# Kernel tuning notes

Measured on AMD Instinct MI355X. Metric: run time of the kernel, lower is better.

The kernel has to match this reference:

```python
import jax, jax.numpy as jnp
import numpy as np

H = 16      # num_heads
HD = 64     # head_dim
W = 1024    # local window size
G = 256     # number of global tokens
EPS = 1e-6
NEG = -1e30


def setup_inputs() -> dict:
    key = jax.random.key(0)
    ks = jax.random.split(key, 7)
    B, S, D = 1, 8192, 1024
    inner = H * HD
    s = 0.02
    return {
        "x": jax.random.normal(ks[0], (B, S, D), jnp.float32),
        "norm_w": jnp.ones((D,), jnp.float32),
        "w_q": jax.random.normal(ks[1], (D, inner), jnp.float32) * s,
        "w_k": jax.random.normal(ks[2], (D, inner), jnp.float32) * s,
        "w_v": jax.random.normal(ks[3], (D, inner), jnp.float32) * s,
        "w_out": jax.random.normal(ks[4], (inner, D), jnp.float32) * s,
        "scorer_w": jax.random.normal(ks[5], (D, 1), jnp.float32) * s,
        "scorer_b": jnp.zeros((1,), jnp.float32),
    }


def reference(x, norm_w, w_q, w_k, w_v, w_out, scorer_w, scorer_b):
    B, S, D = x.shape
    # pre-norm (RMSNorm)
    h = x * jax.lax.rsqrt(jnp.mean(x * x, axis=-1, keepdims=True) + EPS) * norm_w

    def proj(w):  # [B,S,D] -> [B,H,S,HD]
        return jnp.einsum('bsd,de->bse', h, w).reshape(B, S, H, HD).transpose(0, 2, 1, 3)

    q, k, v = proj(w_q), proj(w_k), proj(w_v)
    scale = HD ** -0.5

    # --- local block attention (non-overlapping causal windows) ---
    nW = S // W
    qw = q.reshape(B, H, nW, W, HD)
    kw = k.reshape(B, H, nW, W, HD)
    vw = v.reshape(B, H, nW, W, HD)
    ll = jnp.einsum('bhnqd,bhnkd->bhnqk', qw, kw) * scale  # [B,H,nW,W,W]
    cm = jnp.tril(jnp.ones((W, W), bool))
    ll = jnp.where(cm, ll, NEG).reshape(B, H, S, W)

    # --- sparse global attention over top-G important tokens ---
    scores = (jnp.einsum('bsd,do->bso', h, scorer_w) + scorer_b)[..., 0]  # [B,S]
    _, idx = jax.lax.top_k(scores, G)                                     # [B,G]
    kg = jnp.take_along_axis(k, idx[:, None, :, None], axis=2)            # [B,H,G,HD]
    vg = jnp.take_along_axis(v, idx[:, None, :, None], axis=2)
    lg = jnp.einsum('bhsd,bhgd->bhsg', q, kg) * scale                     # [B,H,S,G]
    pos = jnp.arange(S)
    gmask = idx[:, None, None, :] <= pos[None, None, :, None]             # causal: global pos <= query pos
    lg = jnp.where(gmask, lg, NEG)

    # --- joint softmax over local window + global tokens ---
    attn = jax.nn.softmax(jnp.concatenate([ll, lg], axis=-1), axis=-1)    # [B,H,S,W+G]
    a_loc = attn[..., :W].reshape(B, H, nW, W, W)
    o = jnp.einsum('bhnqk,bhnkd->bhnqd', a_loc, vw).reshape(B, H, S, HD)
    o = o + jnp.einsum('bhsg,bhgd->bhsd', attn[..., W:], vg)

    o = o.transpose(0, 2, 1, 3).reshape(B, S, H * HD)
    return x + jnp.einsum('bse,ed->bsd', o, w_out)  # residual
```

## Files before the change

### kernel.cpp

```cpp
#include <hip/hip_runtime.h>
#include <stdint.h>

#define S_LEN 8192
#define DIM   1024
#define NH    16
#define HD    64
#define WIN   1024
#define GTOK  256
#define QKV_STRIDE (3 * DIM)

typedef __attribute__((ext_vector_type(8))) short bf16x8;
typedef __attribute__((ext_vector_type(4))) float f32x4;
typedef __attribute__((ext_vector_type(16))) float f32x16;
typedef unsigned short u16;
typedef uint32_t u32;

__device__ __forceinline__ u16 f2bf(float f) {
  union { float f; uint32_t u; } v; v.f = f;
  uint32_t r = v.u + 0x7fffu + ((v.u >> 16) & 1u);
  return (u16)(r >> 16);
}
__device__ __forceinline__ float bf2f(u16 b) {
  union { uint32_t u; float f; } v; v.u = ((uint32_t)b) << 16;
  return v.f;
}
__device__ __forceinline__ uint32_t cvtpk(float a, float b) {
  uint32_t r;
  asm("v_cvt_pk_bf16_f32 %0, %1, %2" : "=v"(r) : "v"(a), "v"(b));
  return r;
}

__device__ __forceinline__ void gload_lds16(const void* g, void* l) {
  __builtin_amdgcn_global_load_lds((const __attribute__((address_space(1))) void*)g,
                                   (__attribute__((address_space(3))) void*)l, 16, 0, 0);
}

__global__ __launch_bounds__(256) void rmsnorm_score_kernel(
    const float* __restrict__ x, const float* __restrict__ nw,
    const float* __restrict__ sw, const float* __restrict__ sb,
    u16* __restrict__ h, float* __restrict__ scores) {
  int row = blockIdx.x, tid = threadIdx.x;
  const float4* xr = (const float4*)(x + (size_t)row * DIM);
  float4 v = xr[tid];
  float ss = v.x * v.x + v.y * v.y + v.z * v.z + v.w * v.w;
#pragma unroll
  for (int o = 32; o >= 1; o >>= 1) ss += __shfl_xor(ss, o);
  __shared__ float red[4], red2[4];
  int wv = tid >> 6;
  if ((tid & 63) == 0) red[wv] = ss;
  __syncthreads();
  ss = red[0] + red[1] + red[2] + red[3];
  float rn = rsqrtf(ss * (1.0f / DIM) + 1e-6f);
  float4 w4 = ((const float4*)nw)[tid];
  float h0 = v.x * rn * w4.x, h1 = v.y * rn * w4.y;
  float h2 = v.z * rn * w4.z, h3 = v.w * rn * w4.w;
  uint64_t pack = (uint64_t)f2bf(h0) | ((uint64_t)f2bf(h1) << 16) |
                  ((uint64_t)f2bf(h2) << 32) | ((uint64_t)f2bf(h3) << 48);
  *(uint64_t*)(h + (size_t)row * DIM + tid * 4) = pack;
  float4 s4 = ((const float4*)sw)[tid];
  float sc = h0 * s4.x + h1 * s4.y + h2 * s4.z + h3 * s4.w;
#pragma unroll
  for (int o = 32; o >= 1; o >>= 1) sc += __shfl_xor(sc, o);
  if ((tid & 63) == 0) red2[wv] = sc;
  __syncthreads();
  if (tid == 0) scores[row] = red2[0] + red2[1] + red2[2] + red2[3] + sb[0];
}

__global__ __launch_bounds__(256) void transpose_w_kernel(
    const float* __restrict__ wq, const float* __restrict__ wk,
    const float* __restrict__ wv, const float* __restrict__ wo,
    u16* __restrict__ wqkvT, u16* __restrict__ woutT) {
  __shared__ float tile[32][33];
  int z = blockIdx.z;
  const float* src = (z == 0) ? wq : (z == 1) ? wk : (z == 2) ? wv : wo;
  u16* dst = (z < 3) ? (wqkvT + (size_t)z * DIM * DIM) : woutT;
  int tx = threadIdx.x, ty = threadIdx.y;
  int n0 = blockIdx.x * 32, k0 = blockIdx.y * 32;
#pragma unroll
  for (int i = 0; i < 4; i++)
    tile[ty + i * 8][tx] = src[(size_t)(k0 + ty + i * 8) * DIM + n0 + tx];
  __syncthreads();
#pragma unroll
  for (int i = 0; i < 4; i++)
    dst[(size_t)(n0 + ty + i * 8) * DIM + k0 + tx] = f2bf(tile[tx][ty + i * 8]);
}

__global__ __launch_bounds__(256) void topk_init_kernel(int* __restrict__ cnt) {
  cnt[blockIdx.x * 256 + threadIdx.x] = 0;
}

__global__ __launch_bounds__(256) void topk_count_kernel(
    const float* __restrict__ scores, int* __restrict__ cnt) {
  __shared__ float sj[1024];
  int jbase = blockIdx.y * 1024;
  for (int t = threadIdx.x; t < 1024; t += 256) sj[t] = scores[jbase + t];
  __syncthreads();
  int i = blockIdx.x * 256 + threadIdx.x;
  float my = scores[i];
  int c = 0;
  const float4* s4 = (const float4*)sj;
#pragma unroll 4
  for (int j = 0; j < 256; j++) {
    float4 v = s4[j];
    int b = jbase + j * 4;
    c += (v.x > my) || (v.x == my && (b + 0) < i);
    c += (v.y > my) || (v.y == my && (b + 1) < i);
    c += (v.z > my) || (v.z == my && (b + 2) < i);
    c += (v.w > my) || (v.w == my && (b + 3) < i);
  }
  if (c) atomicAdd(&cnt[i], c);
}

__global__ __launch_bounds__(256) void topk_scatter_kernel(
    const int* __restrict__ cnt, int* __restrict__ gidx) {
  int i = blockIdx.x * 256 + threadIdx.x;
  int c = cnt[i];
  if (c < GTOK) gidx[c] = i;
}

__global__ __launch_bounds__(128) void gather_kernel(
    const u16* __restrict__ qkv, const int* __restrict__ gidx,
    u16* __restrict__ kg, u16* __restrict__ vg) {
  int g = blockIdx.x, t = threadIdx.x;
  size_t src = (size_t)gidx[g] * QKV_STRIDE;
  *(bf16x8*)(kg + (size_t)g * DIM + t * 8) = *(const bf16x8*)(qkv + src + DIM + t * 8);
  *(bf16x8*)(vg + (size_t)g * DIM + t * 8) = *(const bf16x8*)(qkv + src + 2 * DIM + t * 8);
}

template <int RESID>
__global__ __launch_bounds__(512, 2) void gemm256_kernel(
    const u16* __restrict__ A, const u16* __restrict__ B,
    u16* __restrict__ Cb, float* __restrict__ Cf, const float* __restrict__ X,
    int M, int N, int K) {
  __shared__ __align__(16) u16 As[3][256 * 64];
  __shared__ __align__(16) u16 Bs[3][128 * 64];
  const int tid = threadIdx.x;
  const int wave = tid >> 6, lane = tid & 63;
  const int l15 = lane & 15, l4 = lane >> 4;
  const int wr = wave >> 1, wc = wave & 1;
  const int mbase = blockIdx.x * 256, nbase = blockIdx.y * 128;
  const int srow = lane >> 3, schunk = lane & 7;
  const int gcol = (schunk ^ srow) * 8;

  auto stage = [&](int tt, int b) {
    const int kt = tt << 6;
#pragma unroll
    for (int l = 0; l < 4; l++) {
      int row = wave * 32 + l * 8;
      gload_lds16(A + (size_t)(mbase + row + srow) * K + kt + gcol, &As[b][row * 64]);
    }
#pragma unroll
    for (int l = 0; l < 2; l++) {
      int row = wave * 16 + l * 8;
      gload_lds16(B + (size_t)(nbase + row + srow) * K + kt + gcol, &Bs[b][row * 64]);
    }
  };

  const int nt = K >> 6;
  f32x4 acc[4][4] = {};

  stage(0, 0);
  stage(1, 1);
  asm volatile("s_waitcnt vmcnt(6)" ::: "memory");
  __builtin_amdgcn_s_barrier();
  __builtin_amdgcn_sched_barrier(0);

  int cur = 0;
  for (int t = 0; t < nt; t++) {
    int pre = cur + 2; if (pre >= 3) pre -= 3;
    if (t + 2 < nt) stage(t + 2, pre);
    const u16* Ab = &As[cur][0];
    const u16* Bb = &Bs[cur][0];
    bf16x8 bfr[4][2], af[4][2];
#pragma unroll
    for (int nf = 0; nf < 4; nf++) {
      int row = wc * 64 + nf * 16 + l15;
#pragma unroll
      for (int kk = 0; kk < 2; kk++)
        bfr[nf][kk] = *(const bf16x8*)(Bb + row * 64 + (((kk * 4 + l4) ^ (l15 & 7)) * 8));
    }
#pragma unroll
    for (int mi = 0; mi < 4; mi++) {
      int row = wr * 64 + mi * 16 + l15;
#pragma unroll
      for (int kk = 0; kk < 2; kk++)
        af[mi][kk] = *(const bf16x8*)(Ab + row * 64 + (((kk * 4 + l4) ^ (l15 & 7)) * 8));
    }
    __builtin_amdgcn_s_setprio(1);
#pragma unroll
    for (int mi = 0; mi < 4; mi++)
#pragma unroll
      for (int nf = 0; nf < 4; nf++)
#pragma unroll
        for (int kk = 0; kk < 2; kk++)
          acc[mi][nf] = __builtin_amdgcn_mfma_f32_16x16x32_bf16(af[mi][kk], bfr[nf][kk],
                                                                acc[mi][nf], 0, 0, 0);
    __builtin_amdgcn_s_setprio(0);
    if (t + 1 < nt) {
      if (t + 2 < nt) asm volatile("s_waitcnt vmcnt(6)" ::: "memory");
      else            asm volatile("s_waitcnt vmcnt(0)" ::: "memory");
      __builtin_amdgcn_s_barrier();
      __builtin_amdgcn_sched_barrier(0);
    }
    cur = (cur + 1 == 3) ? 0 : cur + 1;
  }

#pragma unroll
  for (int mi = 0; mi < 4; mi++) {
#pragma unroll
    for (int nf = 0; nf < 4; nf++) {
#pragma unroll
      for (int r = 0; r < 4; r++) {
        int row = mbase + wr * 64 + mi * 16 + l4 * 4 + r;
        int col = nbase + wc * 64 + nf * 16 + l15;
        float v = acc[mi][nf][r];
        if (RESID) Cf[(size_t)row * N + col] = X[(size_t)row * N + col] + v;
        else       Cb[(size_t)row * N + col] = f2bf(v);
      }
    }
  }
}

__global__ __launch_bounds__(256) void attn_kernel(
    const u16* __restrict__ qkv, const u16* __restrict__ kg,
    const u16* __restrict__ vg, const int* __restrict__ gidx,
    u16* __restrict__ o) {
  __shared__ __align__(16) u16 kT[2][64][72];
  __shared__ __align__(16) u16 vT[2][64][72];
  __shared__ int gposLds[2][64];
  const int tid = threadIdx.x, wave = tid >> 6, lane = tid & 63;
  const int l31 = lane & 31, hi = lane >> 5;
  const int win = blockIdx.x >> 2, pr = blockIdx.x & 3;
  const int wbase = win * WIN;
  const int hoff = blockIdx.y * HD;
  const int ks = (l31 >> 3) & 3;

  const int skey = tid >> 2;
  const int kc0 = (tid & 3) * 2;
  const int kswz = (skey >> 3) & 3;
  const int kp = tid & 31, dblk = tid >> 5;
  const int vcol = kp ^ ((dblk & 3) << 2);

  bf16x8 nk0, nk1, nva, nvb;
  int ng = 0;
  {
    const u16* kb = qkv + (size_t)(wbase + skey) * QKV_STRIDE + DIM + hoff;
    nk0 = *(const bf16x8*)(kb + kc0 * 8);
    nk1 = *(const bf16x8*)(kb + kc0 * 8 + 8);
    const u16* vb = qkv + (size_t)(wbase + 2 * kp) * QKV_STRIDE + 2 * DIM + hoff + dblk * 8;
    nva = *(const bf16x8*)(vb);
    nvb = *(const bf16x8*)(vb + QKV_STRIDE);
  }

  for (int sp = 0; sp < 2; sp++) {
    const int j = sp ? (7 - pr) : pr;
    const int qsbase = wbase + j * 128;
    const int nLocal = (j + 1) * 2;
    const int nTiles = nLocal + GTOK / 64;
    const int qrow = qsbase + wave * 32 + l31;
    const int qwmax = qsbase + wave * 32 + 31;

    bf16x8 qf[4];
    {
      const float SC2 = 0.125f * 1.44269504088896f;
      const u16* qptr = qkv + (size_t)qrow * QKV_STRIDE + hoff + hi * 8;
#pragma unroll
      for (int ksub = 0; ksub < 4; ksub++) {
        bf16x8 raw = *(const bf16x8*)(qptr + ksub * 16);
        bf16x8 sc;
#pragma unroll
        for (int jj = 0; jj < 8; jj++) sc[jj] = (short)f2bf(bf2f((u16)raw[jj]) * SC2);
        qf[ksub] = sc;
      }
    }

    f32x16 acc0 = {}, acc1 = {};
    float mr = -3.0e38f, lr = 0.f;

    __syncthreads();

    for (int t = 0; t < nTiles; t++) {
      const int p = t & 1;
      const bool isLocal = (t < nLocal);
      const int tbase = wbase + t * 64;
      *(bf16x8*)(&kT[p][skey][(kc0 ^ kswz) * 8]) = nk0;
      *(bf16x8*)(&kT[p][skey][((kc0 + 1) ^ kswz) * 8]) = nk1;
#pragma unroll
      for (int jj = 0; jj < 8; jj++) {
        uint32_t pk2 = (u16)nva[jj] | ((uint32_t)(u16)nvb[jj] << 16);
        ((u32*)&vT[p][dblk * 8 + jj][0])[vcol] = pk2;
      }
      if (!isLocal && tid < 64) gposLds[p][tid] = ng;
      {
        const int ntile = t + 1;
        const u16 *ksrc = nullptr, *vsrc = nullptr;
        size_t vstride = QKV_STRIDE;
        if (ntile < nLocal) {
          ksrc = qkv + (size_t)(wbase + ntile * 64 + skey) * QKV_STRIDE + DIM + hoff + kc0 * 8;
          vsrc = qkv + (size_t)(wbase + ntile * 64 + 2 * kp) * QKV_STRIDE + 2 * DIM + hoff + dblk * 8;
        } else if (ntile < nTiles) {
          ksrc = kg + (size_t)((ntile - nLocal) * 64 + skey) * DIM + hoff + kc0 * 8;
          vsrc = vg + (size_t)((ntile - nLocal) * 64 + 2 * kp) * DIM + hoff + dblk * 8;
          vstride = DIM;
          if (tid < 64) ng = gidx[(ntile - nLocal) * 64 + tid];
        } else if (sp == 0) {
          ksrc = qkv + (size_t)(wbase + skey) * QKV_STRIDE + DIM + hoff + kc0 * 8;
          vsrc = qkv + (size_t)(wbase + 2 * kp) * QKV_STRIDE + 2 * DIM + hoff + dblk * 8;
        }
        if (ksrc) {
          nk0 = *(const bf16x8*)(ksrc);
          nk1 = *(const bf16x8*)(ksrc + 8);
          nva = *(const bf16x8*)(vsrc);
          nvb = *(const bf16x8*)(vsrc + vstride);
        }
      }
      asm volatile("s_waitcnt lgkmcnt(0)" ::: "memory");
      __builtin_amdgcn_s_barrier();
      __builtin_amdgcn_sched_barrier(0);

      if (isLocal && tbase > qwmax) continue;

      float sv[32];
      __builtin_amdgcn_s_setprio(1);
#pragma unroll
      for (int kb = 0; kb < 2; kb++) {
        const u16* krow = &kT[p][kb * 32 + l31][0];
        bf16x8 k0 = *(const bf16x8*)(krow + ((hi + 0) ^ ks) * 8);
        bf16x8 k1 = *(const bf16x8*)(krow + ((hi + 2) ^ ks) * 8);
        bf16x8 k2 = *(const bf16x8*)(krow + ((hi + 4) ^ ks) * 8);
        bf16x8 k3 = *(const bf16x8*)(krow + ((hi + 6) ^ ks) * 8);
        f32x16 z = {};
        z = __builtin_amdgcn_mfma_f32_32x32x16_bf16(k0, qf[0], z, 0, 0, 0);
        z = __builtin_amdgcn_mfma_f32_32x32x16_bf16(k1, qf[1], z, 0, 0, 0);
        z = __builtin_amdgcn_mfma_f32_32x32x16_bf16(k2, qf[2], z, 0, 0, 0);
        z = __builtin_amdgcn_mfma_f32_32x32x16_bf16(k3, qf[3], z, 0, 0, 0);
#pragma unroll
        for (int r = 0; r < 16; r++) sv[kb * 16 + r] = z[r];
      }
      __builtin_amdgcn_s_setprio(0);

      if (isLocal) {
        const int lim = qrow - tbase;
        if (lim < 63) {
#pragma unroll
          for (int kb = 0; kb < 2; kb++)
#pragma unroll
            for (int r = 0; r < 16; r++) {
              int crow = kb * 32 + (r & 3) + 8 * (r >> 2) + 4 * hi;
              if (crow > lim) sv[kb * 16 + r] = -3.0e38f;
            }
        }
      } else {
#pragma unroll
        for (int kb = 0; kb < 2; kb++)
#pragma unroll
          for (int r = 0; r < 16; r++) {
            int kpos = gposLds[p][kb * 32 + (r & 3) + 8 * (r >> 2) + 4 * hi];
            if (kpos > qrow) sv[kb * 16 + r] = -3.0e38f;
          }
      }

      float m0 = sv[0], m1 = sv[1], m2 = sv[2], m3 = sv[3];
#pragma unroll
      for (int i = 4; i < 32; i += 4) {
        m0 = fmaxf(m0, sv[i]);     m1 = fmaxf(m1, sv[i + 1]);
        m2 = fmaxf(m2, sv[i + 2]); m3 = fmaxf(m3, sv[i + 3]);
      }
      float vmax = fmaxf(fmaxf(m0, m1), fmaxf(m2, m3));
      vmax = fmaxf(vmax, __shfl_xor(vmax, 32));
      if (__any(vmax > mr + 11.0f)) {
        float mn = fmaxf(mr, vmax);
        float al = exp2f(mr - mn);
        lr *= al;
        mr = mn;
#pragma unroll
        for (int i = 0; i < 16; i++) { acc0[i] *= al; acc1[i] *= al; }
      }
      float s0 = 0.f, s1 = 0.f, s2 = 0.f, s3 = 0.f;
#pragma unroll
      for (int i = 0; i < 32; i += 4) {
        float p0 = exp2f(sv[i] - mr),     p1 = exp2f(sv[i + 1] - mr);
        float p2 = exp2f(sv[i + 2] - mr), p3 = exp2f(sv[i + 3] - mr);
        sv[i] = p0; sv[i + 1] = p1; sv[i + 2] = p2; sv[i + 3] = p3;
        s0 += p0; s1 += p1; s2 += p2; s3 += p3;
      }
      float ps = (s0 + s1) + (s2 + s3);
      ps += __shfl_xor(ps, 32);
      lr += ps;

      bf16x8 pf[4];
#pragma unroll
      for (int q4 = 0; q4 < 4; q4++) {
        int b = q4 * 8;
        uint32_t w0 = cvtpk(sv[b + 0], sv[b + 1]);
        uint32_t w1 = cvtpk(sv[b + 2], sv[b + 3]);
        uint32_t w2 = cvtpk(sv[b + 4], sv[b + 5]);
        uint32_t w3 = cvtpk(sv[b + 6], sv[b + 7]);
        uint32_t w0s = __shfl_xor((int)w0, 32), w2s = __shfl_xor((int)w2, 32);
        uint32_t w1s = __shfl_xor((int)w1, 32), w3s = __shfl_xor((int)w3, 32);
        union { uint32_t w[4]; bf16x8 v; } u;
        u.w[0] = hi ? w2s : w0;
        u.w[1] = hi ? w3s : w1;
        u.w[2] = hi ? w2 : w0s;
        u.w[3] = hi ? w3 : w1s;
        pf[q4] = u.v;
      }

      __builtin_amdgcn_s_setprio(1);
#pragma unroll
      for (int dsel = 0; dsel < 2; dsel++) {
        const u16* vrow = &vT[p][dsel * 32 + l31][0];
        f32x16 a = dsel ? acc1 : acc0;
#pragma unroll
        for (int ksg = 0; ksg < 4; ksg++) {
          bf16x8 vf = *(const bf16x8*)(vrow + (((ksg * 2 + hi) ^ ks) * 8));
          a = __builtin_amdgcn_mfma_f32_32x32x16_bf16(vf, pf[ksg], a, 0, 0, 0);
        }
        if (dsel) acc1 = a; else acc0 = a;
      }
      __builtin_amdgcn_s_setprio(0);
    }

    float inv = 1.0f / lr;
#pragma unroll
    for (int dsel = 0; dsel < 2; dsel++) {
      f32x16 a = dsel ? acc1 : acc0;
#pragma unroll
      for (int g = 0; g < 4; g++) {
        uint64_t pk = (uint64_t)f2bf(a[g * 4 + 0] * inv)
                    | ((uint64_t)f2bf(a[g * 4 + 1] * inv) << 16)
                    | ((uint64_t)f2bf(a[g * 4 + 2] * inv) << 32)
                    | ((uint64_t)f2bf(a[g * 4 + 3] * inv) << 48);
        *(uint64_t*)(o + (size_t)qrow * DIM + hoff + dsel * 32 + g * 8 + 4 * hi) = pk;
      }
    }
  }
}

extern "C" void kernel_launch(void* const* d_in, const int* in_sizes, int n_in,
                              void* d_out, int out_size, void* d_ws, size_t ws_size,
                              hipStream_t stream) {
  const float* x  = (const float*)d_in[0];
  const float* nw = (const float*)d_in[1];
  const float* wq = (const float*)d_in[2];
  const float* wk = (const float*)d_in[3];
  const float* wv = (const float*)d_in[4];
  const float* wo = (const float*)d_in[5];
  const float* sw = (const float*)d_in[6];
  const float* sb = (const float*)d_in[7];
  float* out = (float*)d_out;

  char* ws = (char*)d_ws;
  size_t off = 0;
  auto alloc = [&](size_t b) {
    char* p = ws + off;
    off = (off + b + 255) & ~(size_t)255;
    return p;
  };
  u16*   h      = (u16*)alloc((size_t)S_LEN * DIM * 2);
  u16*   wqkvT  = (u16*)alloc((size_t)3 * DIM * DIM * 2);
  u16*   woutT  = (u16*)alloc((size_t)DIM * DIM * 2);
  u16*   qkv    = (u16*)alloc((size_t)S_LEN * 3 * DIM * 2);
  u16*   obuf   = (u16*)alloc((size_t)S_LEN * DIM * 2);
  float* scores = (float*)alloc((size_t)S_LEN * 4);
  int*   gidx   = (int*)alloc((size_t)GTOK * 4);
  int*   cnt    = (int*)alloc((size_t)S_LEN * 4);
  u16*   kgbuf  = (u16*)alloc((size_t)GTOK * DIM * 2);
  u16*   vgbuf  = (u16*)alloc((size_t)GTOK * DIM * 2);

  transpose_w_kernel<<<dim3(32, 32, 4), dim3(32, 8), 0, stream>>>(wq, wk, wv, wo, wqkvT, woutT);
  rmsnorm_score_kernel<<<dim3(S_LEN), dim3(256), 0, stream>>>(x, nw, sw, sb, h, scores);
  topk_init_kernel<<<dim3(S_LEN / 256), dim3(256), 0, stream>>>(cnt);
  topk_count_kernel<<<dim3(32, 8), dim3(256), 0, stream>>>(scores, cnt);
  topk_scatter_kernel<<<dim3(S_LEN / 256), dim3(256), 0, stream>>>(cnt, gidx);
  gemm256_kernel<0><<<dim3(32, 24), dim3(512), 0, stream>>>(h, wqkvT, qkv, nullptr, nullptr,
                                                            S_LEN, 3 * DIM, DIM);
  gather_kernel<<<dim3(GTOK), dim3(128), 0, stream>>>(qkv, gidx, kgbuf, vgbuf);
  attn_kernel<<<dim3(32, NH), dim3(256), 0, stream>>>(qkv, kgbuf, vgbuf, gidx, obuf);
  gemm256_kernel<1><<<dim3(32, 8), dim3(512), 0, stream>>>(obuf, woutT, nullptr, out, x,
                                                           S_LEN, DIM, DIM);
}
```

Baseline: 255.0 us.

## Widen attention blocks to 512 threads and process one 256-row query chunk per block

The attention kernel now runs 8 waves per block, each block covering a 256-row query chunk of one window and head in a single pass. This replaces the earlier scheme of 4 waves handling two paired 128-row chunks. Block indices are remapped so the chunks with the most causal tiles are scheduled first, and each staged K/V tile is reused by twice as many query waves. In exchange, the K LDS layout loses its XOR swizzle and V is transposed with scalar 16-bit LDS stores, which may add bank conflicts and LDS write cost. Load balance now depends on scheduling order rather than on pairing chunks within a block.

```diff
diff --git a/kernel.cpp b/kernel.cpp
--- a/kernel.cpp
+++ b/kernel.cpp
@@ -221,7 +221,7 @@
   }
 }
 
-__global__ __launch_bounds__(256) void attn_kernel(
+__global__ __launch_bounds__(512) void attn_kernel(
     const u16* __restrict__ qkv, const u16* __restrict__ kg,
     const u16* __restrict__ vg, const int* __restrict__ gidx,
     u16* __restrict__ o) {
@@ -230,209 +230,187 @@
   __shared__ int gposLds[2][64];
   const int tid = threadIdx.x, wave = tid >> 6, lane = tid & 63;
   const int l31 = lane & 31, hi = lane >> 5;
-  const int win = blockIdx.x >> 2, pr = blockIdx.x & 3;
-  const int wbase = win * WIN;
-  const int hoff = blockIdx.y * HD;
-  const int ks = (l31 >> 3) & 3;
-
-  const int skey = tid >> 2;
-  const int kc0 = (tid & 3) * 2;
-  const int kswz = (skey >> 3) & 3;
-  const int kp = tid & 31, dblk = tid >> 5;
-  const int vcol = kp ^ ((dblk & 3) << 2);
-
-  bf16x8 nk0, nk1, nva, nvb;
+
+  const int r = blockIdx.x + 32 * blockIdx.y;
+  const int half = r >> 8, rr = r & 255;
+  const int h = rr >> 4, w8 = rr & 7, jj = (rr >> 3) & 1;
+  const int j = half ? (jj ? 1 : 0) : (jj ? 2 : 3);
+  const int wbase = w8 * WIN;
+  const int hoff = h * HD;
+  const int qsbase = wbase + j * 256;
+  const int nLocal = (j + 1) * 4;
+  const int nTiles = nLocal + GTOK / 64;
+  const int qrow = qsbase + wave * 32 + l31;
+  const int qwmax = qsbase + wave * 32 + 31;
+
+  const int skey = tid >> 3, sd8 = (tid & 7) * 8;
+  const int vcol = skey ^ ((sd8 >> 4) << 4);
+
+  bf16x8 qf[4];
+  {
+    const float SC2 = 0.125f * 1.44269504088896f;
+    const u16* qptr = qkv + (size_t)qrow * QKV_STRIDE + hoff + hi * 8;
+#pragma unroll
+    for (int ks = 0; ks < 4; ks++) {
+      bf16x8 raw = *(const bf16x8*)(qptr + ks * 16);
+      bf16x8 sc;
+#pragma unroll
+      for (int t = 0; t < 8; t++) sc[t] = (short)f2bf(bf2f((u16)raw[t]) * SC2);
+      qf[ks] = sc;
+    }
+  }
+
+  bf16x8 nk, nv;
   int ng = 0;
   {
-    const u16* kb = qkv + (size_t)(wbase + skey) * QKV_STRIDE + DIM + hoff;
-    nk0 = *(const bf16x8*)(kb + kc0 * 8);
-    nk1 = *(const bf16x8*)(kb + kc0 * 8 + 8);
-    const u16* vb = qkv + (size_t)(wbase + 2 * kp) * QKV_STRIDE + 2 * DIM + hoff + dblk * 8;
-    nva = *(const bf16x8*)(vb);
-    nvb = *(const bf16x8*)(vb + QKV_STRIDE);
-  }
-
-  for (int sp = 0; sp < 2; sp++) {
-    const int j = sp ? (7 - pr) : pr;
-    const int qsbase = wbase + j * 128;
-    const int nLocal = (j + 1) * 2;
-    const int nTiles = nLocal + GTOK / 64;
-    const int qrow = qsbase + wave * 32 + l31;
-    const int qwmax = qsbase + wave * 32 + 31;
-
-    bf16x8 qf[4];
+    const u16* base = qkv + (size_t)(wbase + skey) * QKV_STRIDE + hoff + sd8;
+    nk = *(const bf16x8*)(base + DIM);
+    nv = *(const bf16x8*)(base + 2 * DIM);
+  }
+
+  f32x16 acc0 = {}, acc1 = {};
+  float mr = -3.0e38f, lr = 0.f;
+
+  for (int t = 0; t < nTiles; t++) {
+    const int p = t & 1;
+    const bool isLocal = (t < nLocal);
+    const int tbase = wbase + t * 64;
+    *(bf16x8*)(&kT[p][skey][sd8]) = nk;
+#pragma unroll
+    for (int t8 = 0; t8 < 8; t8++) vT[p][sd8 + t8][vcol] = (u16)nv[t8];
+    if (!isLocal && tid < 64) gposLds[p][tid] = ng;
     {
-      const float SC2 = 0.125f * 1.44269504088896f;
-      const u16* qptr = qkv + (size_t)qrow * QKV_STRIDE + hoff + hi * 8;
-#pragma unroll
-      for (int ksub = 0; ksub < 4; ksub++) {
-        bf16x8 raw = *(const bf16x8*)(qptr + ksub * 16);
-        bf16x8 sc;
-#pragma unroll
-        for (int jj = 0; jj < 8; jj++) sc[jj] = (short)f2bf(bf2f((u16)raw[jj]) * SC2);
-        qf[ksub] = sc;
+      const int nt = t + 1;
+      const u16 *ksrc = nullptr, *vsrc = nullptr;
+      if (nt < nLocal) {
+        const u16* base = qkv + (size_t)(wbase + nt * 64 + skey) * QKV_STRIDE + hoff + sd8;
+        ksrc = base + DIM; vsrc = base + 2 * DIM;
+      } else if (nt < nTiles) {
+        size_t grow = (size_t)((nt - nLocal) * 64 + skey) * DIM + hoff + sd8;
+        ksrc = kg + grow; vsrc = vg + grow;
+        if (tid < 64) ng = gidx[(nt - nLocal) * 64 + tid];
       }
-    }
-
-    f32x16 acc0 = {}, acc1 = {};
-    float mr = -3.0e38f, lr = 0.f;
-
-    __syncthreads();
-
-    for (int t = 0; t < nTiles; t++) {
-      const int p = t & 1;
-      const bool isLocal = (t < nLocal);
-      const int tbase = wbase + t * 64;
-      *(bf16x8*)(&kT[p][skey][(kc0 ^ kswz) * 8]) = nk0;
-      *(bf16x8*)(&kT[p][skey][((kc0 + 1) ^ kswz) * 8]) = nk1;
-#pragma unroll
-      for (int jj = 0; jj < 8; jj++) {
-        uint32_t pk2 = (u16)nva[jj] | ((uint32_t)(u16)nvb[jj] << 16);
-        ((u32*)&vT[p][dblk * 8 + jj][0])[vcol] = pk2;
-      }
-      if (!isLocal && tid < 64) gposLds[p][tid] = ng;
-      {
-        const int ntile = t + 1;
-        const u16 *ksrc = nullptr, *vsrc = nullptr;
-        size_t vstride = QKV_STRIDE;
-        if (ntile < nLocal) {
-          ksrc = qkv + (size_t)(wbase + ntile * 64 + skey) * QKV_STRIDE + DIM + hoff + kc0 * 8;
-          vsrc = qkv + (size_t)(wbase + ntile * 64 + 2 * kp) * QKV_STRIDE + 2 * DIM + hoff + dblk * 8;
-        } else if (ntile < nTiles) {
-          ksrc = kg + (size_t)((ntile - nLocal) * 64 + skey) * DIM + hoff + kc0 * 8;
-          vsrc = vg + (size_t)((ntile - nLocal) * 64 + 2 * kp) * DIM + hoff + dblk * 8;
-          vstride = DIM;
-          if (tid < 64) ng = gidx[(ntile - nLocal) * 64 + tid];
-        } else if (sp == 0) {
-          ksrc = qkv + (size_t)(wbase + skey) * QKV_STRIDE + DIM + hoff + kc0 * 8;
-          vsrc = qkv + (size_t)(wbase + 2 * kp) * QKV_STRIDE + 2 * DIM + hoff + dblk * 8;
-        }
-        if (ksrc) {
-          nk0 = *(const bf16x8*)(ksrc);
-          nk1 = *(const bf16x8*)(ksrc + 8);
-          nva = *(const bf16x8*)(vsrc);
-          nvb = *(const bf16x8*)(vsrc + vstride);
-        }
-      }
-      asm volatile("s_waitcnt lgkmcnt(0)" ::: "memory");
-      __builtin_amdgcn_s_barrier();
-      __builtin_amdgcn_sched_barrier(0);
-
-      if (isLocal && tbase > qwmax) continue;
-
-      float sv[32];
-      __builtin_amdgcn_s_setprio(1);
-#pragma unroll
-      for (int kb = 0; kb < 2; kb++) {
-        const u16* krow = &kT[p][kb * 32 + l31][0];
-        bf16x8 k0 = *(const bf16x8*)(krow + ((hi + 0) ^ ks) * 8);
-        bf16x8 k1 = *(const bf16x8*)(krow + ((hi + 2) ^ ks) * 8);
-        bf16x8 k2 = *(const bf16x8*)(krow + ((hi + 4) ^ ks) * 8);
-        bf16x8 k3 = *(const bf16x8*)(krow + ((hi + 6) ^ ks) * 8);
-        f32x16 z = {};
-        z = __builtin_amdgcn_mfma_f32_32x32x16_bf16(k0, qf[0], z, 0, 0, 0);
-        z = __builtin_amdgcn_mfma_f32_32x32x16_bf16(k1, qf[1], z, 0, 0, 0);
-        z = __builtin_amdgcn_mfma_f32_32x32x16_bf16(k2, qf[2], z, 0, 0, 0);
-        z = __builtin_amdgcn_mfma_f32_32x32x16_bf16(k3, qf[3], z, 0, 0, 0);
-#pragma unroll
-        for (int r = 0; r < 16; r++) sv[kb * 16 + r] = z[r];
-      }
-      __builtin_amdgcn_s_setprio(0);
-
-      if (isLocal) {
-        const int lim = qrow - tbase;
-        if (lim < 63) {
-#pragma unroll
-          for (int kb = 0; kb < 2; kb++)
-#pragma unroll
-            for (int r = 0; r < 16; r++) {
-              int crow = kb * 32 + (r & 3) + 8 * (r >> 2) + 4 * hi;
-              if (crow > lim) sv[kb * 16 + r] = -3.0e38f;
-            }
-        }
-      } else {
+      if (ksrc) { nk = *(const bf16x8*)(ksrc); nv = *(const bf16x8*)(vsrc); }
+    }
+    asm volatile("s_waitcnt lgkmcnt(0)" ::: "memory");
+    __builtin_amdgcn_s_barrier();
+    __builtin_amdgcn_sched_barrier(0);
+
+    if (isLocal && tbase > qwmax) continue;
+
+    float sv[32];
+    __builtin_amdgcn_s_setprio(1);
+#pragma unroll
+    for (int kb = 0; kb < 2; kb++) {
+      const u16* krow = &kT[p][kb * 32 + l31][hi * 8];
+      bf16x8 k0 = *(const bf16x8*)(krow);
+      bf16x8 k1 = *(const bf16x8*)(krow + 16);
+      bf16x8 k2 = *(const bf16x8*)(krow + 32);
+      bf16x8 k3 = *(const bf16x8*)(krow + 48);
+      f32x16 z = {};
+      z = __builtin_amdgcn_mfma_f32_32x32x16_bf16(k0, qf[0], z, 0, 0, 0);
+      z = __builtin_amdgcn_mfma_f32_32x32x16_bf16(k1, qf[1], z, 0, 0, 0);
+      z = __builtin_amdgcn_mfma_f32_32x32x16_bf16(k2, qf[2], z, 0, 0, 0);
+      z = __builtin_amdgcn_mfma_f32_32x32x16_bf16(k3, qf[3], z, 0, 0, 0);
+#pragma unroll
+      for (int rg = 0; rg < 16; rg++) sv[kb * 16 + rg] = z[rg];
+    }
+    __builtin_amdgcn_s_setprio(0);
+
+    if (isLocal) {
+      const int lim = qrow - tbase;
+      if (lim < 63) {
 #pragma unroll
         for (int kb = 0; kb < 2; kb++)
 #pragma unroll
-          for (int r = 0; r < 16; r++) {
-            int kpos = gposLds[p][kb * 32 + (r & 3) + 8 * (r >> 2) + 4 * hi];
-            if (kpos > qrow) sv[kb * 16 + r] = -3.0e38f;
+          for (int rg = 0; rg < 16; rg++) {
+            int crow = kb * 32 + (rg & 3) + 8 * (rg >> 2) + 4 * hi;
+            if (crow > lim) sv[kb * 16 + rg] = -3.0e38f;
           }
       }
-
-      float m0 = sv[0], m1 = sv[1], m2 = sv[2], m3 = sv[3];
-#pragma unroll
-      for (int i = 4; i < 32; i += 4) {
-        m0 = fmaxf(m0, sv[i]);     m1 = fmaxf(m1, sv[i + 1]);
-        m2 = fmaxf(m2, sv[i + 2]); m3 = fmaxf(m3, sv[i + 3]);
+    } else {
+#pragma unroll
+      for (int kb = 0; kb < 2; kb++)
+#pragma unroll
+        for (int rg = 0; rg < 16; rg++) {
+          int kpos = gposLds[p][kb * 32 + (rg & 3) + 8 * (rg >> 2) + 4 * hi];
+          if (kpos > qrow) sv[kb * 16 + rg] = -3.0e38f;
+        }
+    }
+
+    float m0 = sv[0], m1 = sv[1], m2 = sv[2], m3 = sv[3];
+#pragma unroll
+    for (int i = 4; i < 32; i += 4) {
+      m0 = fmaxf(m0, sv[i]);     m1 = fmaxf(m1, sv[i + 1]);
+      m2 = fmaxf(m2, sv[i + 2]); m3 = fmaxf(m3, sv[i + 3]);
+    }
+    float vmax = fmaxf(fmaxf(m0, m1), fmaxf(m2, m3));
+    vmax = fmaxf(vmax, __shfl_xor(vmax, 32));
+    if (__any(vmax > mr + 11.0f)) {
+      float mn = fmaxf(mr, vmax);
+      float al = exp2f(mr - mn);
+      lr *= al;
+      mr = mn;
+#pragma unroll
+      for (int i = 0; i < 16; i++) { acc0[i] *= al; acc1[i] *= al; }
+    }
+    float s0 = 0.f, s1 = 0.f, s2 = 0.f, s3 = 0.f;
+#pragma unroll
+    for (int i = 0; i < 32; i += 4) {
+      float p0 = exp2f(sv[i] - mr),     p1 = exp2f(sv[i + 1] - mr);
+      float p2 = exp2f(sv[i + 2] - mr), p3 = exp2f(sv[i + 3] - mr);
+      sv[i] = p0; sv[i + 1] = p1; sv[i + 2] = p2; sv[i + 3] = p3;
+      s0 += p0; s1 += p1; s2 += p2; s3 += p3;
+    }
+    float ps = (s0 + s1) + (s2 + s3);
+    ps += __shfl_xor(ps, 32);
+    lr += ps;
+
+    bf16x8 pf[4];
+#pragma unroll
+    for (int q4 = 0; q4 < 4; q4++) {
+      int b = q4 * 8;
+      uint32_t w0 = cvtpk(sv[b + 0], sv[b + 1]);
+      uint32_t w1 = cvtpk(sv[b + 2], sv[b + 3]);
+      uint32_t w2 = cvtpk(sv[b + 4], sv[b + 5]);
+      uint32_t w3 = cvtpk(sv[b + 6], sv[b + 7]);
+      uint32_t w0s = __shfl_xor((int)w0, 32), w2s = __shfl_xor((int)w2, 32);
+      uint32_t w1s = __shfl_xor((int)w1, 32), w3s = __shfl_xor((int)w3, 32);
+      union { uint32_t w[4]; bf16x8 v; } u;
+      u.w[0] = hi ? w2s : w0;
+      u.w[1] = hi ? w3s : w1;
+      u.w[2] = hi ? w2 : w0s;
+      u.w[3] = hi ? w3 : w1s;
+      pf[q4] = u.v;
+    }
+
+    __builtin_amdgcn_s_setprio(1);
+#pragma unroll
+    for (int dblk = 0; dblk < 2; dblk++) {
+      const int swz = (dblk * 2 + (l31 >> 4)) << 4;
+      const u16* vrow = &vT[p][dblk * 32 + l31][0];
+      f32x16 a = dblk ? acc1 : acc0;
+#pragma unroll
+      for (int ksg = 0; ksg < 4; ksg++) {
+        bf16x8 vf = *(const bf16x8*)(vrow + ((ksg * 16 + hi * 8) ^ swz));
+        a = __builtin_amdgcn_mfma_f32_32x32x16_bf16(vf, pf[ksg], a, 0, 0, 0);
       }
-      float vmax = fmaxf(fmaxf(m0, m1), fmaxf(m2, m3));
-      vmax = fmaxf(vmax, __shfl_xor(vmax, 32));
-      if (__any(vmax > mr + 11.0f)) {
-        float mn = fmaxf(mr, vmax);
-        float al = exp2f(mr - mn);
-        lr *= al;
-        mr = mn;
-#pragma unroll
-        for (int i = 0; i < 16; i++) { acc0[i] *= al; acc1[i] *= al; }
-      }
-      float s0 = 0.f, s1 = 0.f, s2 = 0.f, s3 = 0.f;
-#pragma unroll
-      for (int i = 0; i < 32; i += 4) {
-        float p0 = exp2f(sv[i] - mr),     p1 = exp2f(sv[i + 1] - mr);
-        float p2 = exp2f(sv[i + 2] - mr), p3 = exp2f(sv[i + 3] - mr);
-        sv[i] = p0; sv[i + 1] = p1; sv[i + 2] = p2; sv[i + 3] = p3;
-        s0 += p0; s1 += p1; s2 += p2; s3 += p3;
-      }
-      float ps = (s0 + s1) + (s2 + s3);
-      ps += __shfl_xor(ps, 32);
-      lr += ps;
-
-      bf16x8 pf[4];
-#pragma unroll
-      for (int q4 = 0; q4 < 4; q4++) {
-        int b = q4 * 8;
-        uint32_t w0 = cvtpk(sv[b + 0], sv[b + 1]);
-        uint32_t w1 = cvtpk(sv[b + 2], sv[b + 3]);
-        uint32_t w2 = cvtpk(sv[b + 4], sv[b + 5]);
-        uint32_t w3 = cvtpk(sv[b + 6], sv[b + 7]);
-        uint32_t w0s = __shfl_xor((int)w0, 32), w2s = __shfl_xor((int)w2, 32);
-        uint32_t w1s = __shfl_xor((int)w1, 32), w3s = __shfl_xor((int)w3, 32);
-        union { uint32_t w[4]; bf16x8 v; } u;
-        u.w[0] = hi ? w2s : w0;
-        u.w[1] = hi ? w3s : w1;
-        u.w[2] = hi ? w2 : w0s;
-        u.w[3] = hi ? w3 : w1s;
-        pf[q4] = u.v;
-      }
-
-      __builtin_amdgcn_s_setprio(1);
-#pragma unroll
-      for (int dsel = 0; dsel < 2; dsel++) {
-        const u16* vrow = &vT[p][dsel * 32 + l31][0];
-        f32x16 a = dsel ? acc1 : acc0;
-#pragma unroll
-        for (int ksg = 0; ksg < 4; ksg++) {
-          bf16x8 vf = *(const bf16x8*)(vrow + (((ksg * 2 + hi) ^ ks) * 8));
-          a = __builtin_amdgcn_mfma_f32_32x32x16_bf16(vf, pf[ksg], a, 0, 0, 0);
-        }
-        if (dsel) acc1 = a; else acc0 = a;
-      }
-      __builtin_amdgcn_s_setprio(0);
-    }
-
-    float inv = 1.0f / lr;
-#pragma unroll
-    for (int dsel = 0; dsel < 2; dsel++) {
-      f32x16 a = dsel ? acc1 : acc0;
-#pragma unroll
-      for (int g = 0; g < 4; g++) {
-        uint64_t pk = (uint64_t)f2bf(a[g * 4 + 0] * inv)
-                    | ((uint64_t)f2bf(a[g * 4 + 1] * inv) << 16)
-                    | ((uint64_t)f2bf(a[g * 4 + 2] * inv) << 32)
-                    | ((uint64_t)f2bf(a[g * 4 + 3] * inv) << 48);
-        *(uint64_t*)(o + (size_t)qrow * DIM + hoff + dsel * 32 + g * 8 + 4 * hi) = pk;
-      }
+      if (dblk) acc1 = a; else acc0 = a;
+    }
+    __builtin_amdgcn_s_setprio(0);
+  }
+
+  float inv = 1.0f / lr;
+#pragma unroll
+  for (int dblk = 0; dblk < 2; dblk++) {
+    f32x16 a = dblk ? acc1 : acc0;
+#pragma unroll
+    for (int g = 0; g < 4; g++) {
+      uint64_t pk = (uint64_t)f2bf(a[g * 4 + 0] * inv)
+                  | ((uint64_t)f2bf(a[g * 4 + 1] * inv) << 16)
+                  | ((uint64_t)f2bf(a[g * 4 + 2] * inv) << 32)
+                  | ((uint64_t)f2bf(a[g * 4 + 3] * inv) << 48);
+      *(uint64_t*)(o + (size_t)qrow * DIM + hoff + dblk * 32 + g * 8 + 4 * hi) = pk;
     }
   }
 }
@@ -476,7 +454,7 @@
   gemm256_kernel<0><<<dim3(32, 24), dim3(512), 0, stream>>>(h, wqkvT, qkv, nullptr, nullptr,
                                                             S_LEN, 3 * DIM, DIM);
   gather_kernel<<<dim3(GTOK), dim3(128), 0, stream>>>(qkv, gidx, kgbuf, vgbuf);
-  attn_kernel<<<dim3(32, NH), dim3(256), 0, stream>>>(qkv, kgbuf, vgbuf, gidx, obuf);
+  attn_kernel<<<dim3(32, NH), dim3(512), 0, stream>>>(qkv, kgbuf, vgbuf, gidx, obuf);
   gemm256_kernel<1><<<dim3(32, 8), dim3(512), 0, stream>>>(obuf, woutT, nullptr, out, x,
                                                            S_LEN, DIM, DIM);
 }
```

Result: faster. 228.6 us (-10.4%).
